# Optimization experiments

Measured on AMD Instinct MI355X. Metric: run time of the kernel, lower is better.

The kernel has to match this reference:

```python
import jax, jax.numpy as jnp
import numpy as np

EMBED_DIM = 768
NUM_HEADS = 12
HEAD_DIM = EMBED_DIM // NUM_HEADS


def setup_inputs() -> dict:
    key = jax.random.key(0)
    ks = jax.random.split(key, 5)
    B, N, D = 8, 1024, EMBED_DIM
    s = 1.0 / np.sqrt(D)
    return {
        "x": jax.random.normal(ks[0], (B, N, D), dtype=jnp.float32),
        "qkv_w": jax.random.uniform(ks[1], (D, 3 * D), jnp.float32, -s, s),  # [in, out]
        "qkv_b": jax.random.uniform(ks[2], (3 * D,), jnp.float32, -s, s),
        "proj_w": jax.random.uniform(ks[3], (D, D), jnp.float32, -s, s),
        "proj_b": jax.random.uniform(ks[4], (D,), jnp.float32, -s, s),
    }


def reference(x, qkv_w, qkv_b, proj_w, proj_b):
    B, N, D = x.shape
    H, Hd = NUM_HEADS, HEAD_DIM
    qkv = x @ qkv_w + qkv_b                          # [B, N, 3D]
    qkv = qkv.reshape(B, N, 3, H, Hd)
    q, k, v = (jnp.moveaxis(qkv, 2, 0)[i].transpose(0, 2, 1, 3) for i in range(3))  # each [B, H, N, Hd]
    scores = jnp.einsum("bhnd,bhmd->bhnm", q, k) / np.sqrt(Hd).astype(x.dtype)
    attn = jax.nn.softmax(scores, axis=-1)           # dropout rate 0.0 -> identity
    out = jnp.einsum("bhnm,bhmd->bhnd", attn, v)     # [B, H, N, Hd]
    out = out.transpose(0, 2, 1, 3).reshape(B, N, D)
    return out @ proj_w + proj_b
```

## Files before the change

### kernel.cpp

```cpp
#include <hip/hip_runtime.h>
#include <hip/hip_bf16.h>

typedef __attribute__((ext_vector_type(8))) short short8;
typedef __attribute__((ext_vector_type(4))) float f32x4;
typedef __attribute__((ext_vector_type(2))) unsigned int uint2v;
typedef __attribute__((ext_vector_type(4))) unsigned int uint4v;
typedef unsigned int u32;

#define QSCALE 0.1803368801111204f

__device__ inline ushort f2bf(float f) {
    unsigned int i = __builtin_bit_cast(unsigned int, f);
    unsigned int r = (i + 0x7FFFu + ((i >> 16) & 1u)) >> 16;
    return (ushort)r;
}
__device__ inline u32 pack_bf16(float a, float b) {
    float2 f2; f2.x = a; f2.y = b;
    __hip_bfloat162 h = __float22bfloat162_rn(f2);
    u32 r; __builtin_memcpy(&r, &h, 4);
    return r;
}

__device__ __forceinline__ void gload_lds16(const ushort* g, ushort* l) {
    __builtin_amdgcn_global_load_lds(
        (const __attribute__((address_space(1))) u32*)g,
        (__attribute__((address_space(3))) u32*)l, 16, 0, 0);
}

__global__ __launch_bounds__(256) void convert_f32_bf16(
    const float* __restrict__ in, ushort* __restrict__ outp, int n8)
{
    int idx = blockIdx.x * 256 + threadIdx.x;
    if (idx >= n8) return;
    const float4 u0 = *(const float4*)&in[(size_t)idx * 8];
    const float4 u1 = *(const float4*)&in[(size_t)idx * 8 + 4];
    uint2v a, b;
    a.x = pack_bf16(u0.x, u0.y); a.y = pack_bf16(u0.z, u0.w);
    b.x = pack_bf16(u1.x, u1.y); b.y = pack_bf16(u1.z, u1.w);
    *(uint2v*)&outp[(size_t)idx * 8] = a;
    *(uint2v*)&outp[(size_t)idx * 8 + 4] = b;
}

__global__ __launch_bounds__(256) void transpose_f32_bf16(
    const float* __restrict__ W, ushort* __restrict__ Wt, int K, int N)
{
    __shared__ float tile[32][33];
    const int n0 = blockIdx.x * 32;
    const int k0 = blockIdx.y * 32;
    const int tx = threadIdx.x & 31;
    const int ty = threadIdx.x >> 5;
    for (int i = ty; i < 32; i += 8)
        tile[i][tx] = W[(size_t)(k0 + i) * N + n0 + tx];
    __syncthreads();
    for (int i = ty; i < 32; i += 8)
        Wt[(size_t)(n0 + i) * K + k0 + tx] = f2bf(tile[tx][i]);
}

template <bool OUT_FP32, bool QKV_MODE>
__global__ __launch_bounds__(256) void gemm_bt(
    const ushort* __restrict__ A, const ushort* __restrict__ Bt,
    const float* __restrict__ bias, void* __restrict__ C,
    ushort* __restrict__ Vt, int M, int N, int K, int ldc)
{
    __shared__ __attribute__((aligned(16))) ushort As[128][64];
    __shared__ __attribute__((aligned(16))) ushort Bs[128][64];
    const int tid  = threadIdx.x;
    const int lane = tid & 63;
    const int w    = tid >> 6;
    const int wm   = (w >> 1) * 64;
    const int wn   = (w & 1) * 64;
    const int g    = lane >> 4;
    const int t    = lane & 15;
    const int m0   = blockIdx.x * 128;
    const int n0   = blockIdx.y * 128;

    const int lr = lane >> 3;
    const int pc = lane & 7;

    f32x4 acc[4][4];
#pragma unroll
    for (int i = 0; i < 4; i++)
#pragma unroll
        for (int j = 0; j < 4; j++) acc[i][j] = {0.f, 0.f, 0.f, 0.f};

    const int xorc = t & 7;

    for (int k0 = 0; k0 < K; k0 += 64) {
#pragma unroll
        for (int p = 0; p < 4; p++) {
            const int row = w * 32 + p * 8 + lr;
            const int gc  = pc ^ (row & 7);
            gload_lds16(&A[(size_t)(m0 + row) * K + k0 + gc * 8], &As[w * 32 + p * 8][0]);
            gload_lds16(&Bt[(size_t)(n0 + row) * K + k0 + gc * 8], &Bs[w * 32 + p * 8][0]);
        }
        __syncthreads();
#pragma unroll
        for (int s = 0; s < 2; s++) {
            short8 a[4], b[4];
            const int ca = ((s * 4 + g) ^ xorc) * 8;
#pragma unroll
            for (int i = 0; i < 4; i++)
                a[i] = *(const short8*)&As[wm + i * 16 + t][ca];
#pragma unroll
            for (int j = 0; j < 4; j++)
                b[j] = *(const short8*)&Bs[wn + j * 16 + t][ca];
#pragma unroll
            for (int i = 0; i < 4; i++)
#pragma unroll
                for (int j = 0; j < 4; j++)
                    acc[i][j] = __builtin_amdgcn_mfma_f32_16x16x32_bf16(
                        a[i], b[j], acc[i][j], 0, 0, 0);
        }
        __syncthreads();
    }

#pragma unroll
    for (int j = 0; j < 4; j++) {
        int col = n0 + wn + j * 16 + t;
        float bv = bias[col];
        if (QKV_MODE && col >= 1536) {
            int h = (col - 1536) >> 6, d = col & 63;
#pragma unroll
            for (int i = 0; i < 4; i++) {
                int n = m0 + wm + i * 16 + g * 4;
                int bb = n >> 10, nn = n & 1023;
                uint2v u;
                u.x = pack_bf16(acc[i][j][0] + bv, acc[i][j][1] + bv);
                u.y = pack_bf16(acc[i][j][2] + bv, acc[i][j][3] + bv);
                *(uint2v*)&Vt[(((size_t)bb * 12 + h) * 64 + d) * 1024 + nn] = u;
            }
        } else {
#pragma unroll
            for (int i = 0; i < 4; i++)
#pragma unroll
                for (int r = 0; r < 4; r++) {
                    int row = m0 + wm + i * 16 + g * 4 + r;
                    float val = acc[i][j][r] + bv;
                    if (QKV_MODE && col < 768) val *= QSCALE;
                    if (OUT_FP32) ((float*)C)[(size_t)row * ldc + col] = val;
                    else          ((ushort*)C)[(size_t)row * ldc + col] = f2bf(val);
                }
        }
    }
}

__global__ __launch_bounds__(256) void gemm_bt2(
    const ushort* __restrict__ A, const ushort* __restrict__ Bt,
    const float* __restrict__ bias, float* __restrict__ C,
    int M, int N, int K, int ldc)
{
    __shared__ __attribute__((aligned(16))) ushort As[64][64];
    __shared__ __attribute__((aligned(16))) ushort Bs[128][64];
    const int tid  = threadIdx.x;
    const int lane = tid & 63;
    const int w    = tid >> 6;
    const int g    = lane >> 4;
    const int t    = lane & 15;
    const int m0   = blockIdx.x * 64;
    const int n0   = blockIdx.y * 128;
    const int wn   = w * 32;

    const int lr = lane >> 3;
    const int pc = lane & 7;

    f32x4 acc[4][2];
#pragma unroll
    for (int i = 0; i < 4; i++)
#pragma unroll
        for (int j = 0; j < 2; j++) acc[i][j] = {0.f, 0.f, 0.f, 0.f};

    const int xorc = t & 7;

    for (int k0 = 0; k0 < K; k0 += 64) {
#pragma unroll
        for (int p = 0; p < 2; p++) {
            const int row = w * 16 + p * 8 + lr;
            const int gc  = pc ^ (row & 7);
            gload_lds16(&A[(size_t)(m0 + row) * K + k0 + gc * 8], &As[w * 16 + p * 8][0]);
        }
#pragma unroll
        for (int p = 0; p < 4; p++) {
            const int row = w * 32 + p * 8 + lr;
            const int gc  = pc ^ (row & 7);
            gload_lds16(&Bt[(size_t)(n0 + row) * K + k0 + gc * 8], &Bs[w * 32 + p * 8][0]);
        }
        __syncthreads();
#pragma unroll
        for (int s = 0; s < 2; s++) {
            short8 a[4], b[2];
            const int ca = ((s * 4 + g) ^ xorc) * 8;
#pragma unroll
            for (int i = 0; i < 4; i++)
                a[i] = *(const short8*)&As[i * 16 + t][ca];
#pragma unroll
            for (int j = 0; j < 2; j++)
                b[j] = *(const short8*)&Bs[wn + j * 16 + t][ca];
#pragma unroll
            for (int i = 0; i < 4; i++)
#pragma unroll
                for (int j = 0; j < 2; j++)
                    acc[i][j] = __builtin_amdgcn_mfma_f32_16x16x32_bf16(
                        a[i], b[j], acc[i][j], 0, 0, 0);
        }
        __syncthreads();
    }

#pragma unroll
    for (int j = 0; j < 2; j++) {
        int col = n0 + wn + j * 16 + t;
        float bv = bias[col];
#pragma unroll
        for (int i = 0; i < 4; i++)
#pragma unroll
            for (int r = 0; r < 4; r++) {
                int row = m0 + i * 16 + g * 4 + r;
                C[(size_t)row * ldc + col] = acc[i][j][r] + bv;
            }
    }
}

__global__ __launch_bounds__(256) void attn_kernel(
    const ushort* __restrict__ qk, const ushort* __restrict__ Vt,
    ushort* __restrict__ out)
{
    __shared__ __attribute__((aligned(16))) ushort Ks[2][64][64];
    __shared__ __attribute__((aligned(16))) ushort Vs[2][64][64];

    const int tid  = threadIdx.x;
    const int lane = tid & 63;
    const int w    = tid >> 6;
    const int g    = lane >> 4;
    const int t    = lane & 15;
    const int bh   = blockIdx.x;
    const int b    = bh / 12;
    const int h    = bh - b * 12;
    const int q0   = blockIdx.y * 128;

    const int srow = tid >> 3;
    const int pc   = tid & 7;
    const size_t base  = (size_t)b * 1024 * 1536;
    const size_t vbase = ((size_t)b * 12 + h) * 64 * 1024;

    short8 qfrag[2][2];
#pragma unroll
    for (int qf = 0; qf < 2; qf++)
#pragma unroll
        for (int s = 0; s < 2; s++)
            qfrag[qf][s] = *(const short8*)&qk[base +
                (size_t)(q0 + qf * 64 + w * 16 + t) * 1536 + h * 64 + s * 32 + g * 8];

#pragma unroll
    for (int p = 0; p < 2; p++) {
        int r = srow + 32 * p;
        int c = (pc ^ (r & 7)) * 8;
        *(short8*)&Ks[0][r][c] =
            *(const short8*)&qk[base + (size_t)r * 1536 + 768 + h * 64 + pc * 8];
        *(short8*)&Vs[0][r][c] =
            *(const short8*)&Vt[vbase + (size_t)r * 1024 + pc * 8];
    }
    __syncthreads();

    f32x4 o_acc[2][4];
#pragma unroll
    for (int qf = 0; qf < 2; qf++)
#pragma unroll
        for (int j = 0; j < 4; j++) o_acc[qf][j] = {0.f, 0.f, 0.f, 0.f};
    float l_part[2] = {0.f, 0.f};

    for (int kt = 0; kt < 16; kt++) {
        const int cur = kt & 1;

        short8 kpre[2], vpre[2];
        if (kt < 15) {
            const int kb = (kt + 1) * 64;
#pragma unroll
            for (int p = 0; p < 2; p++) {
                int r = srow + 32 * p;
                kpre[p] = *(const short8*)&qk[base + (size_t)(kb + r) * 1536 + 768 + h * 64 + pc * 8];
                vpre[p] = *(const short8*)&Vt[vbase + (size_t)r * 1024 + kb + pc * 8];
            }
        }

        short8 kf[2][4], bv[2][4];
#pragma unroll
        for (int s = 0; s < 2; s++)
#pragma unroll
            for (int j = 0; j < 4; j++) {
                const int row = j * 16 + t;
                const int c = ((s * 4 + g) ^ (t & 7)) * 8;
                kf[s][j] = *(const short8*)&Ks[cur][row][c];
                bv[s][j] = *(const short8*)&Vs[cur][row][c];
            }

#pragma unroll
        for (int qf = 0; qf < 2; qf++) {
            f32x4 s_acc[4];
#pragma unroll
            for (int j = 0; j < 4; j++) s_acc[j] = {0.f, 0.f, 0.f, 0.f};
#pragma unroll
            for (int s = 0; s < 2; s++)
#pragma unroll
                for (int j = 0; j < 4; j++)
                    s_acc[j] = __builtin_amdgcn_mfma_f32_16x16x32_bf16(
                        kf[s][j], qfrag[qf][s], s_acc[j], 0, 0, 0);

            u32 wj[4][2];
#pragma unroll
            for (int j = 0; j < 4; j++) {
                float p0 = exp2f(s_acc[j][0]);
                float p1 = exp2f(s_acc[j][1]);
                float p2 = exp2f(s_acc[j][2]);
                float p3 = exp2f(s_acc[j][3]);
                l_part[qf] += (p0 + p1) + (p2 + p3);
                wj[j][0] = pack_bf16(p0, p1);
                wj[j][1] = pack_bf16(p2, p3);
            }

#pragma unroll
            for (int s = 0; s < 2; s++) {
                auto r0 = __builtin_amdgcn_permlane32_swap(wj[2 * s][0], wj[2 * s + 1][0], false, false);
                auto r1 = __builtin_amdgcn_permlane32_swap(wj[2 * s][1], wj[2 * s + 1][1], false, false);
                auto m02 = __builtin_amdgcn_permlane16_swap(r0[0], r0[1], false, false);
                auto m13 = __builtin_amdgcn_permlane16_swap(r1[0], r1[1], false, false);
                uint4v av;
                av.x = m02[0];
                av.y = m13[0];
                av.z = m02[1];
                av.w = m13[1];
                short8 a = __builtin_bit_cast(short8, av);
#pragma unroll
                for (int j = 0; j < 4; j++)
                    o_acc[qf][j] = __builtin_amdgcn_mfma_f32_16x16x32_bf16(
                        a, bv[s][j], o_acc[qf][j], 0, 0, 0);
            }
        }

        if (kt < 15) {
#pragma unroll
            for (int p = 0; p < 2; p++) {
                int r = srow + 32 * p;
                int c = (pc ^ (r & 7)) * 8;
                *(short8*)&Ks[cur ^ 1][r][c] = kpre[p];
                *(short8*)&Vs[cur ^ 1][r][c] = vpre[p];
            }
        }
        __syncthreads();
    }

#pragma unroll
    for (int qf = 0; qf < 2; qf++) {
        float l_tot = l_part[qf];
        l_tot += __shfl_xor(l_tot, 16);
        l_tot += __shfl_xor(l_tot, 32);
        float il[4];
#pragma unroll
        for (int r = 0; r < 4; r++) il[r] = 1.0f / __shfl(l_tot, g * 4 + r);
#pragma unroll
        for (int r = 0; r < 4; r++) {
            int row = q0 + qf * 64 + w * 16 + g * 4 + r;
#pragma unroll
            for (int j = 0; j < 4; j++)
                out[((size_t)(b * 1024 + row)) * 768 + h * 64 + j * 16 + t] =
                    f2bf(o_acc[qf][j][r] * il[r]);
        }
    }
}

extern "C" void kernel_launch(void* const* d_in, const int* in_sizes, int n_in,
                              void* d_out, int out_size, void* d_ws, size_t ws_size,
                              hipStream_t stream)
{
    const float* x      = (const float*)d_in[0];
    const float* qkv_w  = (const float*)d_in[1];
    const float* qkv_b  = (const float*)d_in[2];
    const float* proj_w = (const float*)d_in[3];
    const float* proj_b = (const float*)d_in[4];
    float* out = (float*)d_out;

    char* ws = (char*)d_ws;
    ushort* Wt1 = (ushort*)ws;
    ushort* Wt2 = Wt1 + (size_t)2304 * 768;
    char*   buf = (char*)(Wt2 + (size_t)768 * 768);

    transpose_f32_bf16<<<dim3(72, 24), 256, 0, stream>>>(qkv_w, Wt1, 768, 2304);
    transpose_f32_bf16<<<dim3(24, 24), 256, 0, stream>>>(proj_w, Wt2, 768, 768);

    const size_t wt_bytes   = ((size_t)2304 * 768 + (size_t)768 * 768) * 2;
    const size_t full_bytes = wt_bytes + (size_t)8192 * 768 * 2
                                       + (size_t)8192 * 1536 * 2
                                       + (size_t)8192 * 768 * 2
                                       + (size_t)8192 * 768 * 2;

    if (ws_size >= full_bytes) {
        ushort* xb    = (ushort*)buf;
        ushort* qkO   = xb + (size_t)8192 * 768;
        ushort* VtO   = qkO + (size_t)8192 * 1536;
        ushort* attnO = VtO + (size_t)8192 * 768;
        convert_f32_bf16<<<dim3(3072), 256, 0, stream>>>(x, xb, 786432);
        gemm_bt<false, true><<<dim3(64, 18), 256, 0, stream>>>(
            xb, Wt1, qkv_b, qkO, VtO, 8192, 2304, 768, 1536);
        attn_kernel<<<dim3(96, 8), 256, 0, stream>>>(qkO, VtO, attnO);
        gemm_bt2<<<dim3(128, 6), 256, 0, stream>>>(
            attnO, Wt2, proj_b, out, 8192, 768, 768, 768);
    } else {
        ushort* xbB   = (ushort*)buf;
        ushort* qkB   = xbB + (size_t)1024 * 768;
        ushort* VtB   = qkB + (size_t)1024 * 1536;
        ushort* attnB = VtB + (size_t)1024 * 768;
        for (int b = 0; b < 8; b++) {
            const float* xp = x + (size_t)b * 1024 * 768;
            float* outb = out + (size_t)b * 1024 * 768;
            convert_f32_bf16<<<dim3(384), 256, 0, stream>>>(xp, xbB, 98304);
            gemm_bt<false, true><<<dim3(8, 18), 256, 0, stream>>>(
                xbB, Wt1, qkv_b, qkB, VtB, 1024, 2304, 768, 1536);
            attn_kernel<<<dim3(12, 8), 256, 0, stream>>>(qkB, VtB, attnB);
            gemm_bt2<<<dim3(16, 6), 256, 0, stream>>>(
                attnB, Wt2, proj_b, outb, 1024, 768, 768, 768);
        }
    }
}
```

Baseline: 197.6 us.

## Load K/V fragments directly from global memory, dropping LDS staging and barriers

The attention kernel stops staging K and V tiles through double-buffered shared memory. Each wave now loads its MFMA operand fragments straight from global memory through per-row pointers that advance each key tile. This removes the LDS writes, the LDS reads and the per-iteration __syncthreads. In exchange, every wave redundantly fetches the same K/V data from global memory or cache, and there is no explicit prefetch to hide load latency.

```diff
diff --git a/kernel.cpp b/kernel.cpp
--- a/kernel.cpp
+++ b/kernel.cpp
@@ -223,9 +223,6 @@
     const ushort* __restrict__ qk, const ushort* __restrict__ Vt,
     ushort* __restrict__ out)
 {
-    __shared__ __attribute__((aligned(16))) ushort Ks[2][64][64];
-    __shared__ __attribute__((aligned(16))) ushort Vs[2][64][64];
-
     const int tid  = threadIdx.x;
     const int lane = tid & 63;
     const int w    = tid >> 6;
@@ -236,8 +233,6 @@
     const int h    = bh - b * 12;
     const int q0   = blockIdx.y * 128;
 
-    const int srow = tid >> 3;
-    const int pc   = tid & 7;
     const size_t base  = (size_t)b * 1024 * 1536;
     const size_t vbase = ((size_t)b * 12 + h) * 64 * 1024;
 
@@ -249,16 +244,13 @@
             qfrag[qf][s] = *(const short8*)&qk[base +
                 (size_t)(q0 + qf * 64 + w * 16 + t) * 1536 + h * 64 + s * 32 + g * 8];
 
-#pragma unroll
-    for (int p = 0; p < 2; p++) {
-        int r = srow + 32 * p;
-        int c = (pc ^ (r & 7)) * 8;
-        *(short8*)&Ks[0][r][c] =
-            *(const short8*)&qk[base + (size_t)r * 1536 + 768 + h * 64 + pc * 8];
-        *(short8*)&Vs[0][r][c] =
-            *(const short8*)&Vt[vbase + (size_t)r * 1024 + pc * 8];
-    }
-    __syncthreads();
+    const ushort* kp[4];
+    const ushort* vp[4];
+#pragma unroll
+    for (int j = 0; j < 4; j++) {
+        kp[j] = qk + base + (size_t)(j * 16 + t) * 1536 + 768 + h * 64 + g * 8;
+        vp[j] = Vt + vbase + (size_t)(j * 16 + t) * 1024 + g * 8;
+    }
 
     f32x4 o_acc[2][4];
 #pragma unroll
@@ -268,29 +260,17 @@
     float l_part[2] = {0.f, 0.f};
 
     for (int kt = 0; kt < 16; kt++) {
-        const int cur = kt & 1;
-
-        short8 kpre[2], vpre[2];
-        if (kt < 15) {
-            const int kb = (kt + 1) * 64;
-#pragma unroll
-            for (int p = 0; p < 2; p++) {
-                int r = srow + 32 * p;
-                kpre[p] = *(const short8*)&qk[base + (size_t)(kb + r) * 1536 + 768 + h * 64 + pc * 8];
-                vpre[p] = *(const short8*)&Vt[vbase + (size_t)r * 1024 + kb + pc * 8];
-            }
-        }
-
         short8 kf[2][4], bv[2][4];
 #pragma unroll
-        for (int s = 0; s < 2; s++)
-#pragma unroll
-            for (int j = 0; j < 4; j++) {
-                const int row = j * 16 + t;
-                const int c = ((s * 4 + g) ^ (t & 7)) * 8;
-                kf[s][j] = *(const short8*)&Ks[cur][row][c];
-                bv[s][j] = *(const short8*)&Vs[cur][row][c];
-            }
+        for (int j = 0; j < 4; j++) {
+#pragma unroll
+            for (int s = 0; s < 2; s++) {
+                kf[s][j] = *(const short8*)(kp[j] + s * 32);
+                bv[s][j] = *(const short8*)(vp[j] + s * 32);
+            }
+        }
+#pragma unroll
+        for (int j = 0; j < 4; j++) { kp[j] += 64 * 1536; vp[j] += 64; }
 
 #pragma unroll
         for (int qf = 0; qf < 2; qf++) {
@@ -334,17 +314,6 @@
                         a, bv[s][j], o_acc[qf][j], 0, 0, 0);
             }
         }
-
-        if (kt < 15) {
-#pragma unroll
-            for (int p = 0; p < 2; p++) {
-                int r = srow + 32 * p;
-                int c = (pc ^ (r & 7)) * 8;
-                *(short8*)&Ks[cur ^ 1][r][c] = kpre[p];
-                *(short8*)&Vs[cur ^ 1][r][c] = vpre[p];
-            }
-        }
-        __syncthreads();
     }
 
 #pragma unroll
```

Measured after the change: 240.9 us. 21.9% more time.

## Halve attention query tile to 64 rows and raise occupancy with setprio

Applied to the files above, without the earlier changes.

Each attention block now handles 64 query rows instead of 128, which halves the Q fragments and output accumulators held in registers. The grid doubles to 1536 blocks, and launch bounds now request 5 waves per SIMD to raise occupancy. The change also wraps the MFMA phases in s_setprio, uses the raw exp2 builtin, and unrolls the KV loop by 2. In exchange, K/V tiles are loaded from global memory into LDS twice as often relative to the compute they feed, so reuse per load drops.

```diff
diff --git a/kernel.cpp b/kernel.cpp
--- a/kernel.cpp
+++ b/kernel.cpp
@@ -219,7 +219,7 @@
     }
 }
 
-__global__ __launch_bounds__(256) void attn_kernel(
+__global__ __launch_bounds__(256, 5) void attn_kernel(
     const ushort* __restrict__ qk, const ushort* __restrict__ Vt,
     ushort* __restrict__ out)
 {
@@ -234,20 +234,18 @@
     const int bh   = blockIdx.x;
     const int b    = bh / 12;
     const int h    = bh - b * 12;
-    const int q0   = blockIdx.y * 128;
+    const int q0   = blockIdx.y * 64;
 
     const int srow = tid >> 3;
     const int pc   = tid & 7;
     const size_t base  = (size_t)b * 1024 * 1536;
     const size_t vbase = ((size_t)b * 12 + h) * 64 * 1024;
 
-    short8 qfrag[2][2];
-#pragma unroll
-    for (int qf = 0; qf < 2; qf++)
-#pragma unroll
-        for (int s = 0; s < 2; s++)
-            qfrag[qf][s] = *(const short8*)&qk[base +
-                (size_t)(q0 + qf * 64 + w * 16 + t) * 1536 + h * 64 + s * 32 + g * 8];
+    short8 qfrag[2];
+#pragma unroll
+    for (int s = 0; s < 2; s++)
+        qfrag[s] = *(const short8*)&qk[base +
+            (size_t)(q0 + w * 16 + t) * 1536 + h * 64 + s * 32 + g * 8];
 
 #pragma unroll
     for (int p = 0; p < 2; p++) {
@@ -260,13 +258,12 @@
     }
     __syncthreads();
 
-    f32x4 o_acc[2][4];
-#pragma unroll
-    for (int qf = 0; qf < 2; qf++)
-#pragma unroll
-        for (int j = 0; j < 4; j++) o_acc[qf][j] = {0.f, 0.f, 0.f, 0.f};
-    float l_part[2] = {0.f, 0.f};
-
+    f32x4 o_acc[4];
+#pragma unroll
+    for (int j = 0; j < 4; j++) o_acc[j] = {0.f, 0.f, 0.f, 0.f};
+    float l_part = 0.f;
+
+#pragma unroll 2
     for (int kt = 0; kt < 16; kt++) {
         const int cur = kt & 1;
 
@@ -292,48 +289,49 @@
                 bv[s][j] = *(const short8*)&Vs[cur][row][c];
             }
 
-#pragma unroll
-        for (int qf = 0; qf < 2; qf++) {
-            f32x4 s_acc[4];
-#pragma unroll
-            for (int j = 0; j < 4; j++) s_acc[j] = {0.f, 0.f, 0.f, 0.f};
-#pragma unroll
-            for (int s = 0; s < 2; s++)
-#pragma unroll
-                for (int j = 0; j < 4; j++)
-                    s_acc[j] = __builtin_amdgcn_mfma_f32_16x16x32_bf16(
-                        kf[s][j], qfrag[qf][s], s_acc[j], 0, 0, 0);
-
-            u32 wj[4][2];
-#pragma unroll
-            for (int j = 0; j < 4; j++) {
-                float p0 = exp2f(s_acc[j][0]);
-                float p1 = exp2f(s_acc[j][1]);
-                float p2 = exp2f(s_acc[j][2]);
-                float p3 = exp2f(s_acc[j][3]);
-                l_part[qf] += (p0 + p1) + (p2 + p3);
-                wj[j][0] = pack_bf16(p0, p1);
-                wj[j][1] = pack_bf16(p2, p3);
-            }
-
-#pragma unroll
-            for (int s = 0; s < 2; s++) {
-                auto r0 = __builtin_amdgcn_permlane32_swap(wj[2 * s][0], wj[2 * s + 1][0], false, false);
-                auto r1 = __builtin_amdgcn_permlane32_swap(wj[2 * s][1], wj[2 * s + 1][1], false, false);
-                auto m02 = __builtin_amdgcn_permlane16_swap(r0[0], r0[1], false, false);
-                auto m13 = __builtin_amdgcn_permlane16_swap(r1[0], r1[1], false, false);
-                uint4v av;
-                av.x = m02[0];
-                av.y = m13[0];
-                av.z = m02[1];
-                av.w = m13[1];
-                short8 a = __builtin_bit_cast(short8, av);
-#pragma unroll
-                for (int j = 0; j < 4; j++)
-                    o_acc[qf][j] = __builtin_amdgcn_mfma_f32_16x16x32_bf16(
-                        a, bv[s][j], o_acc[qf][j], 0, 0, 0);
-            }
-        }
+        f32x4 s_acc[4];
+#pragma unroll
+        for (int j = 0; j < 4; j++) s_acc[j] = {0.f, 0.f, 0.f, 0.f};
+        __builtin_amdgcn_s_setprio(1);
+#pragma unroll
+        for (int s = 0; s < 2; s++)
+#pragma unroll
+            for (int j = 0; j < 4; j++)
+                s_acc[j] = __builtin_amdgcn_mfma_f32_16x16x32_bf16(
+                    kf[s][j], qfrag[s], s_acc[j], 0, 0, 0);
+        __builtin_amdgcn_s_setprio(0);
+
+        u32 wj[4][2];
+#pragma unroll
+        for (int j = 0; j < 4; j++) {
+            float p0 = __builtin_amdgcn_exp2f(s_acc[j][0]);
+            float p1 = __builtin_amdgcn_exp2f(s_acc[j][1]);
+            float p2 = __builtin_amdgcn_exp2f(s_acc[j][2]);
+            float p3 = __builtin_amdgcn_exp2f(s_acc[j][3]);
+            l_part += (p0 + p1) + (p2 + p3);
+            wj[j][0] = pack_bf16(p0, p1);
+            wj[j][1] = pack_bf16(p2, p3);
+        }
+
+        __builtin_amdgcn_s_setprio(1);
+#pragma unroll
+        for (int s = 0; s < 2; s++) {
+            auto r0 = __builtin_amdgcn_permlane32_swap(wj[2 * s][0], wj[2 * s + 1][0], false, false);
+            auto r1 = __builtin_amdgcn_permlane32_swap(wj[2 * s][1], wj[2 * s + 1][1], false, false);
+            auto m02 = __builtin_amdgcn_permlane16_swap(r0[0], r0[1], false, false);
+            auto m13 = __builtin_amdgcn_permlane16_swap(r1[0], r1[1], false, false);
+            uint4v av;
+            av.x = m02[0];
+            av.y = m13[0];
+            av.z = m02[1];
+            av.w = m13[1];
+            short8 a = __builtin_bit_cast(short8, av);
+#pragma unroll
+            for (int j = 0; j < 4; j++)
+                o_acc[j] = __builtin_amdgcn_mfma_f32_16x16x32_bf16(
+                    a, bv[s][j], o_acc[j], 0, 0, 0);
+        }
+        __builtin_amdgcn_s_setprio(0);
 
         if (kt < 15) {
 #pragma unroll
@@ -347,9 +345,8 @@
         __syncthreads();
     }
 
-#pragma unroll
-    for (int qf = 0; qf < 2; qf++) {
-        float l_tot = l_part[qf];
+    {
+        float l_tot = l_part;
         l_tot += __shfl_xor(l_tot, 16);
         l_tot += __shfl_xor(l_tot, 32);
         float il[4];
@@ -357,11 +354,11 @@
         for (int r = 0; r < 4; r++) il[r] = 1.0f / __shfl(l_tot, g * 4 + r);
 #pragma unroll
         for (int r = 0; r < 4; r++) {
-            int row = q0 + qf * 64 + w * 16 + g * 4 + r;
+            int row = q0 + w * 16 + g * 4 + r;
 #pragma unroll
             for (int j = 0; j < 4; j++)
                 out[((size_t)(b * 1024 + row)) * 768 + h * 64 + j * 16 + t] =
-                    f2bf(o_acc[qf][j][r] * il[r]);
+                    f2bf(o_acc[j][r] * il[r]);
         }
     }
 }
@@ -399,7 +396,7 @@
         convert_f32_bf16<<<dim3(3072), 256, 0, stream>>>(x, xb, 786432);
         gemm_bt<false, true><<<dim3(64, 18), 256, 0, stream>>>(
             xb, Wt1, qkv_b, qkO, VtO, 8192, 2304, 768, 1536);
-        attn_kernel<<<dim3(96, 8), 256, 0, stream>>>(qkO, VtO, attnO);
+        attn_kernel<<<dim3(96, 16), 256, 0, stream>>>(qkO, VtO, attnO);
         gemm_bt2<<<dim3(128, 6), 256, 0, stream>>>(
             attnO, Wt2, proj_b, out, 8192, 768, 768, 768);
     } else {
@@ -413,7 +410,7 @@
             convert_f32_bf16<<<dim3(384), 256, 0, stream>>>(xp, xbB, 98304);
             gemm_bt<false, true><<<dim3(8, 18), 256, 0, stream>>>(
                 xbB, Wt1, qkv_b, qkB, VtB, 1024, 2304, 768, 1536);
-            attn_kernel<<<dim3(12, 8), 256, 0, stream>>>(qkB, VtB, attnB);
+            attn_kernel<<<dim3(12, 16), 256, 0, stream>>>(qkB, VtB, attnB);
             gemm_bt2<<<dim3(16, 6), 256, 0, stream>>>(
                 attnB, Wt2, proj_b, outb, 1024, 768, 768, 768);
         }
```

After: 428.6 us. 2.17x slower.
